# Performance work log

Measured on AMD Instinct MI355X. Metric: run time of the kernel, lower is better.

The kernel has to match this reference:

```python
import jax, jax.numpy as jnp
import numpy as np

ALPHA = 1e-4
BETA = 1.0
MAX_STD = 1000.0
MIN_STD = 1.0
B = 8192            # number of ragged segments (batch)
NUM_CLASSES = 2
P = 1_000_000       # size of penalized parameter vector


def setup_inputs() -> dict:
    key = jax.random.key(0)
    k1, k2, k3, k4 = jax.random.split(key, 4)
    # ragged lengths: alternate 1024 / 3072, exact total T = B * 2048
    lengths = np.where(np.arange(B) % 2 == 0, 1024, 3072).astype(np.int32)
    T = int(lengths.sum())  # 16_777_216
    seg = np.repeat(np.arange(B, dtype=np.int32), lengths)
    starts = np.concatenate([[0], np.cumsum(lengths)[:-1]])
    local = np.arange(T, dtype=np.int64) - np.repeat(starts, lengths)
    # get_x: positions (1..len)/len within each segment
    xpos = ((local + 1).astype(np.float64) / np.repeat(lengths, lengths)).astype(np.float32)
    return {
        "logits": jax.random.normal(k1, (B, NUM_CLASSES), jnp.float32),
        "labels": jax.random.randint(k2, (B,), 0, 2, jnp.int32),
        "attention_weights": jax.random.uniform(k3, (T,), jnp.float32),
        "params": jax.random.normal(k4, (P,), jnp.float32),
        "xpos": jnp.asarray(xpos),
        "segment_ids": jnp.asarray(seg),
        "lengths": jnp.asarray(lengths),
    }


def reference(logits, labels, attention_weights, params, xpos, segment_ids, lengths):
    nseg = logits.shape[0]
    lens_f = lengths.astype(jnp.float32)

    # CrossEntropyLoss (mean reduction)
    logp = jax.nn.log_softmax(logits, axis=-1)
    nll = -jnp.mean(jnp.take_along_axis(logp, labels[:, None].astype(jnp.int32), axis=1))

    # --- no-grad block: per-segment mean and ideal-gaussian target r ---
    w = jax.lax.stop_gradient(attention_weights)
    sum_w = jax.ops.segment_sum(w, segment_ids, num_segments=nseg)          # [B]
    mean = jax.ops.segment_sum(xpos * w, segment_ids, num_segments=nseg) / sum_w
    ideal_std = jnp.where(labels == 1, MIN_STD, MAX_STD) / lens_f           # [B]
    mu_t = mean[segment_ids]                                                # [T]
    std_t = ideal_std[segment_ids]                                          # [T]
    z = (xpos - mu_t) / std_t
    r_hat = jnp.exp(-0.5 * z * z) / (std_t * jnp.sqrt(2.0 * jnp.pi))        # normal pdf
    r_sum = jax.ops.segment_sum(r_hat, segment_ids, num_segments=nseg)
    r = r_hat / (r_sum[segment_ids] + 1e-6)
    r = jax.lax.stop_gradient(r)

    # L1 penalty on params
    penalty = ALPHA / 2 * jnp.abs(params).sum()

    # per-segment mean of squared diff, then mean over segments
    diff2 = (attention_weights - r) ** 2
    per_seg = jax.ops.segment_sum(diff2, segment_ids, num_segments=nseg) / lens_f
    awp = BETA / 2 * per_seg.mean()

    loss = nll + penalty + awp
    return jnp.stack([loss, nll])
```

## Files before the change

### kernel.cpp

```cpp
#include <hip/hip_runtime.h>


#define TPB 256
#define PARAM_BLOCKS 256

__device__ __forceinline__ float blockReduceSum(float v, float* sm) {
  #pragma unroll
  for (int off = 32; off > 0; off >>= 1) v += __shfl_down(v, off, 64);
  const int lane = threadIdx.x & 63;
  const int wid  = threadIdx.x >> 6;
  if (lane == 0) sm[wid] = v;
  __syncthreads();
  float s = sm[0] + sm[1] + sm[2] + sm[3];
  __syncthreads();
  return s;
}

__device__ __forceinline__ float2 blockReduceSum2(float a, float b, float* sm) {
  #pragma unroll
  for (int off = 32; off > 0; off >>= 1) {
    a += __shfl_down(a, off, 64);
    b += __shfl_down(b, off, 64);
  }
  const int lane = threadIdx.x & 63;
  const int wid  = threadIdx.x >> 6;
  if (lane == 0) { sm[wid] = a; sm[4 + wid] = b; }
  __syncthreads();
  float2 r;
  r.x = sm[0] + sm[1] + sm[2] + sm[3];
  r.y = sm[4] + sm[5] + sm[6] + sm[7];
  __syncthreads();
  return r;
}

__global__ __launch_bounds__(TPB)
void scan_kernel(const int* __restrict__ lengths, int nseg,
                 int* __restrict__ starts) {
  __shared__ int wsum[4];
  const int t = threadIdx.x;
  const int per = (nseg + TPB - 1) / TPB;
  const int base = t * per;
  int local = 0;
  for (int j = 0; j < per; j++) {
    int idx = base + j;
    if (idx < nseg) local += lengths[idx];
  }
  const int lane = t & 63, wid = t >> 6;
  int incl = local;
  #pragma unroll
  for (int off = 1; off < 64; off <<= 1) {
    int n = __shfl_up(incl, off, 64);
    if (lane >= off) incl += n;
  }
  if (lane == 63) wsum[wid] = incl;
  __syncthreads();
  int wbase = 0;
  for (int i = 0; i < wid; i++) wbase += wsum[i];
  int run = wbase + incl - local;
  for (int j = 0; j < per; j++) {
    int idx = base + j;
    if (idx < nseg) { starts[idx] = run; run += lengths[idx]; }
  }
}

template <int NC>
__device__ __forceinline__ void seg_body(const float4* __restrict__ w4, int start4,
                                         int len, int lab,
                                         float* __restrict__ out_slot, float* sm) {
  const float inv_len = 1.0f / (float)len;
  float4 wv[NC], rv[NC];
  float aw = 0.0f, axw = 0.0f;
  #pragma unroll
  for (int k = 0; k < NC; k++) {
    const int vi = (k << 8) + threadIdx.x;
    wv[k] = w4[start4 + vi];
    const int i0 = vi << 2;
    aw += wv[k].x + wv[k].y + wv[k].z + wv[k].w;
    axw = fmaf((float)(i0 + 1) * inv_len, wv[k].x, axw);
    axw = fmaf((float)(i0 + 2) * inv_len, wv[k].y, axw);
    axw = fmaf((float)(i0 + 3) * inv_len, wv[k].z, axw);
    axw = fmaf((float)(i0 + 4) * inv_len, wv[k].w, axw);
  }
  const float2 s2 = blockReduceSum2(aw, axw, sm);
  const float mean = s2.y / s2.x;
  const float invstd = (float)len * (lab == 1 ? 1.0f : 0.001f);
  const float rn = 0.39894228040143267f * invstd;
  float ar = 0.0f;
  #pragma unroll
  for (int k = 0; k < NC; k++) {
    const int i0 = ((k << 8) + threadIdx.x) << 2;
    float z0 = ((float)(i0 + 1) * inv_len - mean) * invstd;
    float z1 = ((float)(i0 + 2) * inv_len - mean) * invstd;
    float z2 = ((float)(i0 + 3) * inv_len - mean) * invstd;
    float z3 = ((float)(i0 + 4) * inv_len - mean) * invstd;
    rv[k].x = __expf(-0.5f * z0 * z0) * rn;
    rv[k].y = __expf(-0.5f * z1 * z1) * rn;
    rv[k].z = __expf(-0.5f * z2 * z2) * rn;
    rv[k].w = __expf(-0.5f * z3 * z3) * rn;
    ar += rv[k].x + rv[k].y + rv[k].z + rv[k].w;
  }
  const float r_sum = blockReduceSum(ar, sm);
  const float rinv = 1.0f / (r_sum + 1e-6f);
  float ad = 0.0f;
  #pragma unroll
  for (int k = 0; k < NC; k++) {
    float d0 = wv[k].x - rv[k].x * rinv;
    float d1 = wv[k].y - rv[k].y * rinv;
    float d2 = wv[k].z - rv[k].z * rinv;
    float d3 = wv[k].w - rv[k].w * rinv;
    ad = fmaf(d0, d0, ad); ad = fmaf(d1, d1, ad);
    ad = fmaf(d2, d2, ad); ad = fmaf(d3, d3, ad);
  }
  const float dsum = blockReduceSum(ad, sm);
  if (threadIdx.x == 0) *out_slot = dsum * inv_len;
}

__device__ void seg_generic(const float* __restrict__ w, int start, int len, int lab,
                            float* __restrict__ out_slot, float* sm) {
  const float inv_len = 1.0f / (float)len;
  float aw = 0.0f, axw = 0.0f;
  for (int i = threadIdx.x; i < len; i += TPB) {
    float wv = w[start + i];
    aw += wv;
    axw = fmaf((float)(i + 1) * inv_len, wv, axw);
  }
  const float2 s2 = blockReduceSum2(aw, axw, sm);
  const float mean = s2.y / s2.x;
  const float invstd = (float)len * (lab == 1 ? 1.0f : 0.001f);
  const float rn = 0.39894228040143267f * invstd;
  float ar = 0.0f;
  for (int i = threadIdx.x; i < len; i += TPB) {
    float z = ((float)(i + 1) * inv_len - mean) * invstd;
    ar += __expf(-0.5f * z * z) * rn;
  }
  const float r_sum = blockReduceSum(ar, sm);
  const float rinv = 1.0f / (r_sum + 1e-6f);
  float ad = 0.0f;
  for (int i = threadIdx.x; i < len; i += TPB) {
    float z = ((float)(i + 1) * inv_len - mean) * invstd;
    float rh = __expf(-0.5f * z * z) * rn;
    float d = w[start + i] - rh * rinv;
    ad = fmaf(d, d, ad);
  }
  const float dsum = blockReduceSum(ad, sm);
  if (threadIdx.x == 0) *out_slot = dsum * inv_len;
}

__global__ __launch_bounds__(TPB)
void main_kernel(const float* __restrict__ attw, const float* __restrict__ params,
                 const float* __restrict__ logits, const int* __restrict__ labels,
                 const int* __restrict__ lengths, const int* __restrict__ starts,
                 int nseg, int P, float* __restrict__ partial) {
  __shared__ float sm[8];
  const int b = blockIdx.x;
  if (b < nseg) {
    const int len = lengths[b];
    const int start = starts[b];
    const int lab = labels[b];
    if (len == 1024 && (start & 3) == 0)
      seg_body<1>((const float4*)attw, start >> 2, len, lab, &partial[b], sm);
    else if (len == 3072 && (start & 3) == 0)
      seg_body<3>((const float4*)attw, start >> 2, len, lab, &partial[b], sm);
    else
      seg_generic(attw, start, len, lab, &partial[b], sm);
  } else if (b < nseg + PARAM_BLOCKS) {
    const int pb = b - nseg;
    const int P4 = P >> 2;
    const float4* p4 = (const float4*)params;
    float a = 0.0f;
    for (int i = pb * TPB + threadIdx.x; i < P4; i += PARAM_BLOCKS * TPB) {
      float4 v = p4[i];
      a += fabsf(v.x) + fabsf(v.y) + fabsf(v.z) + fabsf(v.w);
    }
    if (pb == 0 && threadIdx.x == 0)
      for (int i = P4 << 2; i < P; i++) a += fabsf(params[i]);
    float tot = blockReduceSum(a, sm);
    if (threadIdx.x == 0) partial[b] = tot;
  } else {
    float acc = 0.0f;
    for (int s = threadIdx.x; s < nseg; s += TPB) {
      float l0 = logits[2 * s], l1 = logits[2 * s + 1];
      int lab = labels[s];
      float m = fmaxf(l0, l1);
      float lse = m + logf(expf(l0 - m) + expf(l1 - m));
      acc += (lab ? l1 : l0) - lse;
    }
    float tot = blockReduceSum(acc, sm);
    if (threadIdx.x == 0) partial[b] = tot;
  }
}

__global__ __launch_bounds__(TPB)
void finalize_kernel(const float* __restrict__ partial, int nseg,
                     float* __restrict__ out) {
  __shared__ float sm[8];
  float a_awp = 0.0f, a_abs = 0.0f;
  for (int i = threadIdx.x; i < nseg; i += TPB) a_awp += partial[i];
  for (int i = nseg + threadIdx.x; i < nseg + PARAM_BLOCKS; i += TPB)
    a_abs += partial[i];
  const float2 s2 = blockReduceSum2(a_awp, a_abs, sm);
  if (threadIdx.x == 0) {
    const float nll = -partial[nseg + PARAM_BLOCKS] / (float)nseg;
    const float penalty = 0.5f * 1e-4f * s2.y;
    const float awp = 0.5f * (s2.x / (float)nseg);
    out[0] = nll + penalty + awp;
    out[1] = nll;
  }
}

extern "C" void kernel_launch(void* const* d_in, const int* in_sizes, int n_in,
                              void* d_out, int out_size, void* d_ws, size_t ws_size,
                              hipStream_t stream) {
  const float* logits  = (const float*)d_in[0];
  const int*   labels  = (const int*)d_in[1];
  const float* attw    = (const float*)d_in[2];
  const float* params  = (const float*)d_in[3];
  const int*   lengths = (const int*)d_in[6];
  const int nseg = in_sizes[1];
  const int P    = in_sizes[3];

  int*   starts  = (int*)d_ws;
  size_t poff    = ((size_t)nseg * sizeof(int) + 255) & ~(size_t)255;
  float* partial = (float*)((char*)d_ws + poff);
  float* out     = (float*)d_out;

  scan_kernel<<<1, TPB, 0, stream>>>(lengths, nseg, starts);
  main_kernel<<<nseg + PARAM_BLOCKS + 1, TPB, 0, stream>>>(
      attw, params, logits, labels, lengths, starts, nseg, P, partial);
  finalize_kernel<<<1, TPB, 0, stream>>>(partial, nseg, out);
}
```

Baseline: 209.0 us.

## Process one segment per wavefront and expand squared difference into running sums

```diff
diff --git a/kernel.cpp b/kernel.cpp
--- a/kernel.cpp
+++ b/kernel.cpp
@@ -3,6 +3,16 @@
 
 #define TPB 256
 #define PARAM_BLOCKS 256
+#define SEGS_PER_BLOCK 4
+
+__device__ __forceinline__ void waveReduce3(float& a, float& b, float& c) {
+  #pragma unroll
+  for (int off = 32; off > 0; off >>= 1) {
+    a += __shfl_xor(a, off, 64);
+    b += __shfl_xor(b, off, 64);
+    c += __shfl_xor(c, off, 64);
+  }
+}
 
 __device__ __forceinline__ float blockReduceSum(float v, float* sm) {
   #pragma unroll
@@ -14,23 +24,6 @@
   float s = sm[0] + sm[1] + sm[2] + sm[3];
   __syncthreads();
   return s;
-}
-
-__device__ __forceinline__ float2 blockReduceSum2(float a, float b, float* sm) {
-  #pragma unroll
-  for (int off = 32; off > 0; off >>= 1) {
-    a += __shfl_down(a, off, 64);
-    b += __shfl_down(b, off, 64);
-  }
-  const int lane = threadIdx.x & 63;
-  const int wid  = threadIdx.x >> 6;
-  if (lane == 0) { sm[wid] = a; sm[4 + wid] = b; }
-  __syncthreads();
-  float2 r;
-  r.x = sm[0] + sm[1] + sm[2] + sm[3];
-  r.y = sm[4] + sm[5] + sm[6] + sm[7];
-  __syncthreads();
-  return r;
 }
 
 __global__ __launch_bounds__(TPB)
@@ -64,15 +57,15 @@
 }
 
 template <int NC>
-__device__ __forceinline__ void seg_body(const float4* __restrict__ w4, int start4,
-                                         int len, int lab,
-                                         float* __restrict__ out_slot, float* sm) {
+__device__ __forceinline__ float seg_wave(const float4* __restrict__ w4,
+                                          int start4, int len, int lab) {
+  const int lane = threadIdx.x & 63;
   const float inv_len = 1.0f / (float)len;
-  float4 wv[NC], rv[NC];
-  float aw = 0.0f, axw = 0.0f;
+  float4 wv[NC];
+  float aw = 0.0f, axw = 0.0f, aww = 0.0f;
   #pragma unroll
   for (int k = 0; k < NC; k++) {
-    const int vi = (k << 8) + threadIdx.x;
+    const int vi = (k << 6) + lane;
     wv[k] = w4[start4 + vi];
     const int i0 = vi << 2;
     aw += wv[k].x + wv[k].y + wv[k].z + wv[k].w;
@@ -80,70 +73,66 @@
     axw = fmaf((float)(i0 + 2) * inv_len, wv[k].y, axw);
     axw = fmaf((float)(i0 + 3) * inv_len, wv[k].z, axw);
     axw = fmaf((float)(i0 + 4) * inv_len, wv[k].w, axw);
-  }
-  const float2 s2 = blockReduceSum2(aw, axw, sm);
-  const float mean = s2.y / s2.x;
+    aww = fmaf(wv[k].x, wv[k].x, aww);
+    aww = fmaf(wv[k].y, wv[k].y, aww);
+    aww = fmaf(wv[k].z, wv[k].z, aww);
+    aww = fmaf(wv[k].w, wv[k].w, aww);
+  }
+  waveReduce3(aw, axw, aww);
+  const float mean = axw / aw;
   const float invstd = (float)len * (lab == 1 ? 1.0f : 0.001f);
   const float rn = 0.39894228040143267f * invstd;
-  float ar = 0.0f;
+  float ar = 0.0f, awr = 0.0f, arr = 0.0f;
   #pragma unroll
   for (int k = 0; k < NC; k++) {
-    const int i0 = ((k << 8) + threadIdx.x) << 2;
+    const int i0 = ((k << 6) + lane) << 2;
     float z0 = ((float)(i0 + 1) * inv_len - mean) * invstd;
     float z1 = ((float)(i0 + 2) * inv_len - mean) * invstd;
     float z2 = ((float)(i0 + 3) * inv_len - mean) * invstd;
     float z3 = ((float)(i0 + 4) * inv_len - mean) * invstd;
-    rv[k].x = __expf(-0.5f * z0 * z0) * rn;
-    rv[k].y = __expf(-0.5f * z1 * z1) * rn;
-    rv[k].z = __expf(-0.5f * z2 * z2) * rn;
-    rv[k].w = __expf(-0.5f * z3 * z3) * rn;
-    ar += rv[k].x + rv[k].y + rv[k].z + rv[k].w;
-  }
-  const float r_sum = blockReduceSum(ar, sm);
-  const float rinv = 1.0f / (r_sum + 1e-6f);
-  float ad = 0.0f;
-  #pragma unroll
-  for (int k = 0; k < NC; k++) {
-    float d0 = wv[k].x - rv[k].x * rinv;
-    float d1 = wv[k].y - rv[k].y * rinv;
-    float d2 = wv[k].z - rv[k].z * rinv;
-    float d3 = wv[k].w - rv[k].w * rinv;
-    ad = fmaf(d0, d0, ad); ad = fmaf(d1, d1, ad);
-    ad = fmaf(d2, d2, ad); ad = fmaf(d3, d3, ad);
-  }
-  const float dsum = blockReduceSum(ad, sm);
-  if (threadIdx.x == 0) *out_slot = dsum * inv_len;
-}
-
-__device__ void seg_generic(const float* __restrict__ w, int start, int len, int lab,
-                            float* __restrict__ out_slot, float* sm) {
+    float r0 = __expf(-0.5f * z0 * z0) * rn;
+    float r1 = __expf(-0.5f * z1 * z1) * rn;
+    float r2 = __expf(-0.5f * z2 * z2) * rn;
+    float r3 = __expf(-0.5f * z3 * z3) * rn;
+    ar += r0 + r1 + r2 + r3;
+    awr = fmaf(wv[k].x, r0, awr); awr = fmaf(wv[k].y, r1, awr);
+    awr = fmaf(wv[k].z, r2, awr); awr = fmaf(wv[k].w, r3, awr);
+    arr = fmaf(r0, r0, arr); arr = fmaf(r1, r1, arr);
+    arr = fmaf(r2, r2, arr); arr = fmaf(r3, r3, arr);
+  }
+  waveReduce3(ar, awr, arr);
+  const float rinv = 1.0f / (ar + 1e-6f);
+  const float dsum = aww - 2.0f * rinv * awr + rinv * rinv * arr;
+  return dsum * inv_len;
+}
+
+__device__ float seg_wave_generic(const float* __restrict__ w, int start,
+                                  int len, int lab) {
+  const int lane = threadIdx.x & 63;
   const float inv_len = 1.0f / (float)len;
-  float aw = 0.0f, axw = 0.0f;
-  for (int i = threadIdx.x; i < len; i += TPB) {
+  float aw = 0.0f, axw = 0.0f, aww = 0.0f;
+  for (int i = lane; i < len; i += 64) {
     float wv = w[start + i];
     aw += wv;
     axw = fmaf((float)(i + 1) * inv_len, wv, axw);
-  }
-  const float2 s2 = blockReduceSum2(aw, axw, sm);
-  const float mean = s2.y / s2.x;
+    aww = fmaf(wv, wv, aww);
+  }
+  waveReduce3(aw, axw, aww);
+  const float mean = axw / aw;
   const float invstd = (float)len * (lab == 1 ? 1.0f : 0.001f);
   const float rn = 0.39894228040143267f * invstd;
-  float ar = 0.0f;
-  for (int i = threadIdx.x; i < len; i += TPB) {
-    float z = ((float)(i + 1) * inv_len - mean) * invstd;
-    ar += __expf(-0.5f * z * z) * rn;
-  }
-  const float r_sum = blockReduceSum(ar, sm);
-  const float rinv = 1.0f / (r_sum + 1e-6f);
-  float ad = 0.0f;
-  for (int i = threadIdx.x; i < len; i += TPB) {
+  float ar = 0.0f, awr = 0.0f, arr = 0.0f;
+  for (int i = lane; i < len; i += 64) {
     float z = ((float)(i + 1) * inv_len - mean) * invstd;
     float rh = __expf(-0.5f * z * z) * rn;
-    float d = w[start + i] - rh * rinv;
-    ad = fmaf(d, d, ad);
-  }
-  const float dsum = blockReduceSum(ad, sm);
-  if (threadIdx.x == 0) *out_slot = dsum * inv_len;
+    ar += rh;
+    awr = fmaf(w[start + i], rh, awr);
+    arr = fmaf(rh, rh, arr);
+  }
+  waveReduce3(ar, awr, arr);
+  const float rinv = 1.0f / (ar + 1e-6f);
+  const float dsum = aww - 2.0f * rinv * awr + rinv * rinv * arr;
+  return dsum * inv_len;
 }
 
 __global__ __launch_bounds__(TPB)
@@ -151,20 +140,27 @@
                  const float* __restrict__ logits, const int* __restrict__ labels,
                  const int* __restrict__ lengths, const int* __restrict__ starts,
                  int nseg, int P, float* __restrict__ partial) {
-  __shared__ float sm[8];
+  __shared__ float sm[4];
   const int b = blockIdx.x;
-  if (b < nseg) {
-    const int len = lengths[b];
-    const int start = starts[b];
-    const int lab = labels[b];
-    if (len == 1024 && (start & 3) == 0)
-      seg_body<1>((const float4*)attw, start >> 2, len, lab, &partial[b], sm);
-    else if (len == 3072 && (start & 3) == 0)
-      seg_body<3>((const float4*)attw, start >> 2, len, lab, &partial[b], sm);
-    else
-      seg_generic(attw, start, len, lab, &partial[b], sm);
-  } else if (b < nseg + PARAM_BLOCKS) {
-    const int pb = b - nseg;
+  const int nsegblk = (nseg + SEGS_PER_BLOCK - 1) / SEGS_PER_BLOCK;
+  if (b < nsegblk) {
+    const int wid = threadIdx.x >> 6;
+    const int seg = b * SEGS_PER_BLOCK + wid;
+    if (seg < nseg) {
+      const int len = lengths[seg];
+      const int start = starts[seg];
+      const int lab = labels[seg];
+      float r;
+      if (len == 1024 && (start & 3) == 0)
+        r = seg_wave<4>((const float4*)attw, start >> 2, len, lab);
+      else if (len == 3072 && (start & 3) == 0)
+        r = seg_wave<12>((const float4*)attw, start >> 2, len, lab);
+      else
+        r = seg_wave_generic(attw, start, len, lab);
+      if ((threadIdx.x & 63) == 0) partial[seg] = r;
+    }
+  } else if (b < nsegblk + PARAM_BLOCKS) {
+    const int pb = b - nsegblk;
     const int P4 = P >> 2;
     const float4* p4 = (const float4*)params;
     float a = 0.0f;
@@ -175,7 +171,7 @@
     if (pb == 0 && threadIdx.x == 0)
       for (int i = P4 << 2; i < P; i++) a += fabsf(params[i]);
     float tot = blockReduceSum(a, sm);
-    if (threadIdx.x == 0) partial[b] = tot;
+    if (threadIdx.x == 0) partial[nseg + pb] = tot;
   } else {
     float acc = 0.0f;
     for (int s = threadIdx.x; s < nseg; s += TPB) {
@@ -186,7 +182,7 @@
       acc += (lab ? l1 : l0) - lse;
     }
     float tot = blockReduceSum(acc, sm);
-    if (threadIdx.x == 0) partial[b] = tot;
+    if (threadIdx.x == 0) partial[nseg + PARAM_BLOCKS] = tot;
   }
 }
 
@@ -196,13 +192,21 @@
   __shared__ float sm[8];
   float a_awp = 0.0f, a_abs = 0.0f;
   for (int i = threadIdx.x; i < nseg; i += TPB) a_awp += partial[i];
-  for (int i = nseg + threadIdx.x; i < nseg + PARAM_BLOCKS; i += TPB)
-    a_abs += partial[i];
-  const float2 s2 = blockReduceSum2(a_awp, a_abs, sm);
+  for (int i = threadIdx.x; i < PARAM_BLOCKS; i += TPB) a_abs += partial[nseg + i];
+  #pragma unroll
+  for (int off = 32; off > 0; off >>= 1) {
+    a_awp += __shfl_down(a_awp, off, 64);
+    a_abs += __shfl_down(a_abs, off, 64);
+  }
+  const int lane = threadIdx.x & 63, wid = threadIdx.x >> 6;
+  if (lane == 0) { sm[wid] = a_awp; sm[4 + wid] = a_abs; }
+  __syncthreads();
   if (threadIdx.x == 0) {
+    float s_awp = sm[0] + sm[1] + sm[2] + sm[3];
+    float s_abs = sm[4] + sm[5] + sm[6] + sm[7];
     const float nll = -partial[nseg + PARAM_BLOCKS] / (float)nseg;
-    const float penalty = 0.5f * 1e-4f * s2.y;
-    const float awp = 0.5f * (s2.x / (float)nseg);
+    const float penalty = 0.5f * 1e-4f * s_abs;
+    const float awp = 0.5f * (s_awp / (float)nseg);
     out[0] = nll + penalty + awp;
     out[1] = nll;
   }
@@ -219,13 +223,14 @@
   const int nseg = in_sizes[1];
   const int P    = in_sizes[3];
 
-  int*   starts  = (int*)d_ws;
-  size_t poff    = ((size_t)nseg * sizeof(int) + 255) & ~(size_t)255;
+  int* starts = (int*)d_ws;
+  size_t poff = ((size_t)nseg * sizeof(int) + 255) & ~(size_t)255;
   float* partial = (float*)((char*)d_ws + poff);
-  float* out     = (float*)d_out;
-
+  float* out = (float*)d_out;
+
+  const int nsegblk = (nseg + SEGS_PER_BLOCK - 1) / SEGS_PER_BLOCK;
   scan_kernel<<<1, TPB, 0, stream>>>(lengths, nseg, starts);
-  main_kernel<<<nseg + PARAM_BLOCKS + 1, TPB, 0, stream>>>(
+  main_kernel<<<nsegblk + PARAM_BLOCKS + 1, TPB, 0, stream>>>(
       attw, params, logits, labels, lengths, starts, nseg, P, partial);
   finalize_kernel<<<1, TPB, 0, stream>>>(partial, nseg, out);
 }
```

New measurement: 211.3 us. Within noise of the previous version (+1.1%).
